# Performance work log

Hardware: AMD Instinct MI355X
Metric: run time of the kernel (lower is better)

## Reference

```python
import jax, jax.numpy as jnp
import numpy as np

N = 8192      # num_nodes (adj.shape[0])
CIN = 32
COUT = 32     # must equal CIN so wd = x @ wp @ x.T is (N, N)
CS = 4        # Chebyshev order, static operator
CD = 4        # Chebyshev order, dynamic operator


def setup_inputs() -> dict:
    key = jax.random.key(0)
    k1, k2, k3, k4, k5 = jax.random.split(key, 5)
    x = jax.random.normal(k1, (N, CIN), jnp.float32)
    # scale ws so its spectral radius is O(1); keeps the Chebyshev recurrence numerically tame
    ws = jax.random.normal(k2, (N, N), jnp.float32) * np.float32(1.0 / np.sqrt(N))
    # small scale on wp so wd = x wp x^T has O(1) entries
    wp = jax.random.normal(k3, (CIN, COUT), jnp.float32) * np.float32(1e-3)
    ts = jax.random.normal(k4, (CS, CIN, COUT), jnp.float32)
    td = jax.random.normal(k5, (CD, CIN, COUT), jnp.float32)
    return {"x": x, "ws": ws, "wp": wp, "ts": ts, "td": td}


def reference(x, ws, wp, ts, td):
    # Static operator: Chebyshev expansion T0 = I, T1 = ws, Tk = 2 ws T_{k-1} - T_{k-2}.
    # Run the recurrence on the propagated features y_k = T_k(ws) @ x  (N, cin)
    # instead of forming the (N, N) polynomial matrices -- same math, far less traffic.
    y0 = x                      # T0 @ x
    y1 = ws @ x                 # T1 @ x
    out = y0 @ ts[0]            # shared k=0 term (added into both branches, as in the source)
    out_s = out + y1 @ ts[1]
    for k in range(2, CS):
        y0, y1 = y1, 2.0 * (ws @ y1) - y0
        out_s = out_s + y1 @ ts[k]
    # Dynamic operator: data-dependent graph wd = x @ wp @ x.T  (N, N)
    wd = (x @ wp) @ x.T
    z0 = x
    z1 = wd @ x
    out_d = out + z1 @ td[1]
    for k in range(2, CD):
        z0, z1 = z1, 2.0 * (wd @ z1) - z0
        out_d = out_d + z1 @ td[k]
    # act_func is None in this configuration
    return out_s + out_d
```

## Files before the change

kernel.cpp:

```cpp
#include <hip/hip_runtime.h>
#include <hip/hip_bf16.h>


typedef __attribute__((ext_vector_type(8))) short short8;
typedef __attribute__((ext_vector_type(4))) float floatx4;

constexpr int NSPLIT = 8;

__device__ inline unsigned short f2bf(float f) {
    union { float f; unsigned u; } v; v.f = f;
    unsigned r = v.u + 0x7FFFu + ((v.u >> 16) & 1u);
    return (unsigned short)(r >> 16);
}

__device__ inline floatx4 ntload4(const float* p) {
    return __builtin_nontemporal_load((const floatx4*)p);
}

__global__ __launch_bounds__(256) void k_prep(const float* __restrict__ x,
                                              const float* __restrict__ wp,
                                              float* __restrict__ xp,
                                              float* __restrict__ Gpart,
                                              unsigned short* __restrict__ Vb) {
    __shared__ float sx[8192];
    __shared__ float swp[1024];
    __shared__ unsigned short st[32][264];
    const int t = threadIdx.x;
    const int n0 = blockIdx.x * 256;
    const floatx4* x4 = (const floatx4*)(x + (size_t)n0 * 32);
    floatx4* sx4 = (floatx4*)sx;
#pragma unroll
    for (int i = 0; i < 8; ++i) sx4[i * 256 + t] = x4[i * 256 + t];
    for (int i = t; i < 1024; i += 256) swp[i] = wp[i];
    __syncthreads();

    float row[32];
#pragma unroll
    for (int a = 0; a < 32; ++a) row[a] = sx[t * 32 + a];

    float* xpr = xp + (size_t)(n0 + t) * 32;
#pragma unroll
    for (int c = 0; c < 32; ++c) {
        float s = 0.f;
#pragma unroll
        for (int a = 0; a < 32; ++a) s += row[a] * swp[a * 32 + c];
        xpr[c] = s;
        st[c][t] = f2bf(row[c]);
    }

    const int a = t >> 3;
    const int b = 4 * (t & 7);
    float g0 = 0.f, g1 = 0.f, g2 = 0.f, g3 = 0.f;
    for (int i = 0; i < 256; ++i) {
        float va = sx[i * 32 + a];
        floatx4 vb = *(floatx4*)&sx[i * 32 + b];
        g0 += va * vb.x; g1 += va * vb.y; g2 += va * vb.z; g3 += va * vb.w;
    }
    floatx4 g = {g0, g1, g2, g3};
    *(floatx4*)&Gpart[(size_t)blockIdx.x * 1024 + (size_t)(a * 32 + b)] = g;

    __syncthreads();
    const int lane = t & 63, wv = t >> 6;
    const int l15 = lane & 15, l4 = lane >> 4;
    short8* Vb8 = (short8*)Vb;
#pragma unroll
    for (int q = 0; q < 4; ++q) {
        int idx = wv * 4 + q;
        int c8 = idx >> 1, h = idx & 1;
        short8 v = *(const short8*)&st[h * 16 + l15][c8 * 32 + l4 * 8];
        Vb8[((size_t)(n0 / 32 + c8) * 2 + h) * 64 + lane] = v;
    }
}

__global__ void k_coef(const float* __restrict__ Gpart, const float* __restrict__ wp,
                       const float* __restrict__ ts, const float* __restrict__ td,
                       float* __restrict__ Cx, float* __restrict__ Cxp) {
    __shared__ float G[1024], W[1024], H1[1024], H2[1024];
    __shared__ float swp[1024], td1[1024], td2[1024], td3[1024], ts0[1024];
    int t = threadIdx.x;
    int a = t >> 5, b = t & 31;
    float gs = 0.f;
    for (int p = 0; p < 32; ++p) gs += Gpart[p * 1024 + t];
    G[t] = gs; swp[t] = wp[t]; ts0[t] = ts[t];
    td1[t] = td[1024 + t]; td2[t] = td[2048 + t]; td3[t] = td[3072 + t];
    __syncthreads();
    float s = 0.f;
    for (int c = 0; c < 32; ++c) s += G[a * 32 + c] * swp[c * 32 + b];
    W[t] = s; __syncthreads();
    s = 0.f;
    for (int c = 0; c < 32; ++c) s += W[a * 32 + c] * G[c * 32 + b];
    H1[t] = s; __syncthreads();
    s = 0.f;
    for (int c = 0; c < 32; ++c) s += W[a * 32 + c] * H1[c * 32 + b];
    H2[t] = 2.f * s - G[t]; __syncthreads();
    s = 0.f;
    for (int c = 0; c < 32; ++c)
        s += G[a * 32 + c] * td1[c * 32 + b]
           + 2.f * H1[a * 32 + c] * td2[c * 32 + b]
           + (2.f * H2[a * 32 + c] - G[a * 32 + c]) * td3[c * 32 + b];
    Cxp[t] = s;
    Cx[t] = 2.f * ts0[t] - td2[t];
}

__global__ __launch_bounds__(256) void k_gemm1(const float* __restrict__ A,
                                               unsigned short* __restrict__ wsb,
                                               const unsigned short* __restrict__ Vb,
                                               float* __restrict__ Ypart) {
    __shared__ unsigned short sbuf[4][16 * 256];
    const int t = threadIdx.x;
    const int lane = t & 63;
    const int wv = t >> 6;
    const int l15 = lane & 15;
    const int l4 = lane >> 4;
    const int bx = blockIdx.x, by = blockIdx.y;
    const int k0 = by * 1024;
    const int kc0 = by * 32;
    const int rowbase = bx * 64 + wv * 16;

    unsigned short* wout =
        wsb + (((size_t)(bx * NSPLIT + by) * 8192) + (size_t)wv * 64 + lane) * 8;
    const short8* Vb8 = (const short8*)Vb;
    unsigned short* mybuf = sbuf[wv];
    const int wchunk = lane >> 1, whalf = lane & 1;

    floatx4 acc0 = {0.f, 0.f, 0.f, 0.f};
    floatx4 acc1 = {0.f, 0.f, 0.f, 0.f};

    for (int s = 0; s < 4; ++s) {
        const int ks = k0 + s * 256;
#pragma unroll
        for (int r = 0; r < 16; ++r) {
            floatx4 f = ntload4(A + (size_t)(rowbase + r) * 8192 + ks + lane * 4);
            ushort4 h;
            h.x = f2bf(f.x); h.y = f2bf(f.y); h.z = f2bf(f.z); h.w = f2bf(f.w);
            *(ushort4*)(mybuf + r * 256 + ((wchunk ^ r) * 8 + whalf * 4)) = h;
        }
#pragma unroll 4
        for (int kk = 0; kk < 8; ++kk) {
            short8 av = *(short8*)(mybuf + l15 * 256 + (((kk * 4 + l4) ^ l15) * 8));
            const int kc = kc0 + s * 8 + kk;
            short8 b0 = Vb8[((size_t)kc * 2 + 0) * 64 + lane];
            short8 b1 = Vb8[((size_t)kc * 2 + 1) * 64 + lane];
            *(short8*)(wout + (size_t)(s * 8 + kk) * 2048) = av;
            acc0 = __builtin_amdgcn_mfma_f32_16x16x32_bf16(av, b0, acc0, 0, 0, 0);
            acc1 = __builtin_amdgcn_mfma_f32_16x16x32_bf16(av, b1, acc1, 0, 0, 0);
        }
    }
    float* yp = Ypart + (size_t)by * 262144;
    const int row0 = bx * 64 + wv * 16 + l4 * 4;
#pragma unroll
    for (int r = 0; r < 4; ++r) {
        yp[(size_t)(row0 + r) * 32 + l15] = acc0[r];
        yp[(size_t)(row0 + r) * 32 + 16 + l15] = acc1[r];
    }
}

__global__ __launch_bounds__(256) void k_gemm2(const unsigned short* __restrict__ wsb,
                                               const unsigned short* __restrict__ Vb,
                                               float* __restrict__ Ypart) {
    const int t = threadIdx.x;
    const int lane = t & 63;
    const int wv = t >> 6;
    const int l15 = lane & 15;
    const int l4 = lane >> 4;
    const int bx = blockIdx.x, by = blockIdx.y;
    const int kc0 = by * 32;

    const short8* win = (const short8*)wsb
        + ((size_t)(bx * NSPLIT + by) * 8192) + (size_t)wv * 64 + lane;
    const short8* Vb8 = (const short8*)Vb;

    floatx4 acc0 = {0.f, 0.f, 0.f, 0.f};
    floatx4 acc1 = {0.f, 0.f, 0.f, 0.f};

#pragma unroll 8
    for (int c = 0; c < 32; ++c) {
        short8 av = win[(size_t)c * 256];
        short8 b0 = Vb8[((size_t)(kc0 + c) * 2 + 0) * 64 + lane];
        short8 b1 = Vb8[((size_t)(kc0 + c) * 2 + 1) * 64 + lane];
        acc0 = __builtin_amdgcn_mfma_f32_16x16x32_bf16(av, b0, acc0, 0, 0, 0);
        acc1 = __builtin_amdgcn_mfma_f32_16x16x32_bf16(av, b1, acc1, 0, 0, 0);
    }
    float* yp = Ypart + (size_t)by * 262144;
    const int row0 = bx * 64 + wv * 16 + l4 * 4;
#pragma unroll
    for (int r = 0; r < 4; ++r) {
        yp[(size_t)(row0 + r) * 32 + l15] = acc0[r];
        yp[(size_t)(row0 + r) * 32 + 16 + l15] = acc1[r];
    }
}

__global__ __launch_bounds__(256) void k_trans(const float* __restrict__ Ypart,
                                               const float* __restrict__ prev,
                                               float alpha, float beta,
                                               float* __restrict__ y,
                                               unsigned short* __restrict__ Vb) {
    __shared__ unsigned short st[32][264];
    const int t = threadIdx.x;
    const int n0 = blockIdx.x * 256;
    const size_t base4 = (size_t)n0 * 8;
    floatx4 r[8];
#pragma unroll
    for (int j = 0; j < 8; ++j) r[j] = {0.f, 0.f, 0.f, 0.f};
    for (int p = 0; p < NSPLIT; ++p) {
        const float* P = Ypart + (size_t)p * 262144;
#pragma unroll
        for (int j = 0; j < 8; ++j)
            r[j] += ntload4(P + (base4 + j * 256 + t) * 4);
    }
    const floatx4* prev4 = (const floatx4*)prev;
    floatx4* y4 = (floatx4*)y;
#pragma unroll
    for (int j = 0; j < 8; ++j) {
        floatx4 pv = prev4[base4 + j * 256 + t];
        floatx4 v;
        v.x = alpha * r[j].x + beta * pv.x;
        v.y = alpha * r[j].y + beta * pv.y;
        v.z = alpha * r[j].z + beta * pv.z;
        v.w = alpha * r[j].w + beta * pv.w;
        y4[base4 + j * 256 + t] = v;
        int q = j * 256 + t;
        int lr = q >> 3;
        int c4 = (q & 7) * 4;
        st[c4 + 0][lr] = f2bf(v.x);
        st[c4 + 1][lr] = f2bf(v.y);
        st[c4 + 2][lr] = f2bf(v.z);
        st[c4 + 3][lr] = f2bf(v.w);
    }
    __syncthreads();
    const int lane = t & 63, wv = t >> 6;
    const int l15 = lane & 15, l4 = lane >> 4;
    short8* Vb8 = (short8*)Vb;
#pragma unroll
    for (int q = 0; q < 4; ++q) {
        int idx = wv * 4 + q;
        int c8 = idx >> 1, h = idx & 1;
        short8 v = *(const short8*)&st[h * 16 + l15][c8 * 32 + l4 * 8];
        Vb8[((size_t)(n0 / 32 + c8) * 2 + h) * 64 + lane] = v;
    }
}

__global__ void k_final(const float* __restrict__ x, const float* __restrict__ xp,
                        const float* __restrict__ y1, const float* __restrict__ y2,
                        const float* __restrict__ y3, const float* __restrict__ Cx,
                        const float* __restrict__ Cxp, const float* __restrict__ ts,
                        float* __restrict__ out) {
    __shared__ float m0[1024], m1[1024], m2[1024], m3[1024], m4[1024];
    int t = threadIdx.x;
    for (int i = t; i < 1024; i += 256) {
        m0[i] = Cx[i]; m1[i] = Cxp[i];
        m2[i] = ts[1024 + i]; m3[i] = ts[2048 + i]; m4[i] = ts[3072 + i];
    }
    __syncthreads();
    int g = blockIdx.x * 256 + t;
    int n = g >> 5, c = g & 31;
    const float* xr  = x  + (size_t)n * 32;
    const float* xpr = xp + (size_t)n * 32;
    const float* y1r = y1 + (size_t)n * 32;
    const float* y2r = y2 + (size_t)n * 32;
    const float* y3r = y3 + (size_t)n * 32;
    float s = 0.f;
#pragma unroll
    for (int a = 0; a < 32; ++a) {
        s += xr[a]  * m0[a * 32 + c]
           + xpr[a] * m1[a * 32 + c]
           + y1r[a] * m2[a * 32 + c]
           + y2r[a] * m3[a * 32 + c]
           + y3r[a] * m4[a * 32 + c];
    }
    out[g] = s;
}

extern "C" void kernel_launch(void* const* d_in, const int* in_sizes, int n_in,
                              void* d_out, int out_size, void* d_ws, size_t ws_size,
                              hipStream_t stream) {
    const float* x  = (const float*)d_in[0];
    const float* ws = (const float*)d_in[1];
    const float* wp = (const float*)d_in[2];
    const float* ts = (const float*)d_in[3];
    const float* td = (const float*)d_in[4];
    float* out = (float*)d_out;

    char* w = (char*)d_ws;
    unsigned short* wsb = (unsigned short*)w;
    float* Ppart = (float*)(w + 134217728);
    float* xp  = Ppart + (size_t)NSPLIT * 262144;
    float* y1  = xp + 262144;
    float* y2  = y1 + 262144;
    float* y3  = y2 + 262144;
    unsigned short* Vb = (unsigned short*)(y3 + 262144);
    float* Gpart = (float*)(Vb + 262144);
    float* Cx  = Gpart + 32768;
    float* Cxp = Cx + 1024;

    dim3 gg(128, NSPLIT);
    k_prep<<<32, 256, 0, stream>>>(x, wp, xp, Gpart, Vb);
    k_coef<<<1, 1024, 0, stream>>>(Gpart, wp, ts, td, Cx, Cxp);
    k_gemm1<<<gg, 256, 0, stream>>>(ws, wsb, Vb, Ppart);
    k_trans<<<32, 256, 0, stream>>>(Ppart, x, 1.0f, 0.0f, y1, Vb);
    k_gemm2<<<gg, 256, 0, stream>>>(wsb, Vb, Ppart);
    k_trans<<<32, 256, 0, stream>>>(Ppart, x, 2.0f, -1.0f, y2, Vb);
    k_gemm2<<<gg, 256, 0, stream>>>(wsb, Vb, Ppart);
    k_trans<<<32, 256, 0, stream>>>(Ppart, y1, 2.0f, -1.0f, y3, Vb);

    k_final<<<1024, 256, 0, stream>>>(x, xp, y1, y2, y3, Cx, Cxp, ts, out);
}
```

Measured before the change: 481.6 us.

## Fuse pipeline into one cooperative persistent kernel holding ws tiles in registers

Replaces the nine-kernel sequence with a single cooperative kernel of 1024 blocks that converts its ws tile to bf16 once and keeps it in registers (32 short8 per lane) across all three propagation passes, separated by grid-wide syncs. This removes the 128 MB bf16 copy of ws written to and re-read from global memory, and removes the per-kernel launch gaps. It costs heavy register pressure at 4 blocks per CU, requires all 1024 blocks to be co-resident, and adds grid-sync latency. The old multi-kernel path is kept as a fallback if the cooperative launch fails.

```diff
diff --git a/kernel.cpp b/kernel.cpp
--- a/kernel.cpp
+++ b/kernel.cpp
@@ -1,6 +1,8 @@
 #include <hip/hip_runtime.h>
-#include <hip/hip_bf16.h>
-
+#include <hip/hip_cooperative_groups.h>
+
+
+namespace cg = cooperative_groups;
 
 typedef __attribute__((ext_vector_type(8))) short short8;
 typedef __attribute__((ext_vector_type(4))) float floatx4;
@@ -15,6 +17,235 @@
 
 __device__ inline floatx4 ntload4(const float* p) {
     return __builtin_nontemporal_load((const floatx4*)p);
+}
+
+struct __align__(16) SMem {
+    union {
+        unsigned short sbuf[4][16 * 256];
+        struct { float swp[1024]; unsigned short st[32][136]; } prep;
+        struct { float G[1024], W[1024], H1[1024], H2[1024]; } coef;
+        unsigned short st16[32][48];
+        float fin[5][1024];
+    };
+};
+
+__global__ __launch_bounds__(256, 4) void k_all(
+    const float* __restrict__ x, const float* __restrict__ ws,
+    const float* __restrict__ wp, const float* __restrict__ ts,
+    const float* __restrict__ td, float* __restrict__ out,
+    float* __restrict__ xp, float* __restrict__ y1,
+    float* __restrict__ y2, float* __restrict__ y3,
+    unsigned short* __restrict__ Vb0, unsigned short* __restrict__ Vb1,
+    unsigned short* __restrict__ Vb2, float* __restrict__ Yp,
+    float* __restrict__ Gpart, float* __restrict__ Cx, float* __restrict__ Cxp)
+{
+    cg::grid_group grid = cg::this_grid();
+    __shared__ SMem sm;
+    const int t = threadIdx.x;
+    const int lane = t & 63, wv = t >> 6, l15 = lane & 15, l4 = lane >> 4;
+    const int bid = blockIdx.x;
+    const int bx = bid >> 3, by = bid & 7;
+    const int k0 = by * 1024, kc0 = by * 32;
+    const int rowbase = bx * 64 + wv * 16;
+
+    if (bid < 64) {
+        const int n0 = bid * 128;
+        for (int i = t; i < 1024; i += 256) sm.prep.swp[i] = wp[i];
+        __syncthreads();
+        if (t < 128) {
+            const float* xr = x + (size_t)(n0 + t) * 32;
+            float row[32];
+#pragma unroll
+            for (int a = 0; a < 32; ++a) row[a] = xr[a];
+            float* xpr = xp + (size_t)(n0 + t) * 32;
+#pragma unroll
+            for (int c = 0; c < 32; ++c) {
+                float s = 0.f;
+#pragma unroll
+                for (int a = 0; a < 32; ++a) s += row[a] * sm.prep.swp[a * 32 + c];
+                xpr[c] = s;
+                sm.prep.st[c][t] = f2bf(row[c]);
+            }
+        }
+        {
+            const int a = t >> 3, b4 = 4 * (t & 7);
+            float g0 = 0.f, g1 = 0.f, g2 = 0.f, g3 = 0.f;
+            for (int i = 0; i < 128; ++i) {
+                float va = x[(size_t)(n0 + i) * 32 + a];
+                floatx4 vb = *(const floatx4*)&x[(size_t)(n0 + i) * 32 + b4];
+                g0 += va * vb.x; g1 += va * vb.y; g2 += va * vb.z; g3 += va * vb.w;
+            }
+            floatx4 g = {g0, g1, g2, g3};
+            *(floatx4*)&Gpart[(size_t)bid * 1024 + (size_t)(a * 32 + b4)] = g;
+        }
+        __syncthreads();
+        short8* Vb8 = (short8*)Vb0;
+#pragma unroll
+        for (int q = 0; q < 2; ++q) {
+            int idx = wv * 2 + q;
+            int c8 = idx >> 1, h = idx & 1;
+            short8 v = *(const short8*)&sm.prep.st[h * 16 + l15][c8 * 32 + l4 * 8];
+            Vb8[((size_t)(n0 / 32 + c8) * 2 + h) * 64 + lane] = v;
+        }
+        __syncthreads();
+    }
+
+    short8 wreg[32];
+    {
+        unsigned short* mybuf = sm.sbuf[wv];
+        const int wchunk = lane >> 1, whalf = lane & 1;
+#pragma unroll
+        for (int s = 0; s < 4; ++s) {
+            const int ks = k0 + s * 256;
+#pragma unroll
+            for (int r = 0; r < 16; ++r) {
+                floatx4 f = ntload4(ws + (size_t)(rowbase + r) * 8192 + ks + lane * 4);
+                ushort4 h;
+                h.x = f2bf(f.x); h.y = f2bf(f.y); h.z = f2bf(f.z); h.w = f2bf(f.w);
+                *(ushort4*)(mybuf + r * 256 + ((wchunk ^ r) * 8 + whalf * 4)) = h;
+            }
+#pragma unroll
+            for (int kk = 0; kk < 8; ++kk)
+                wreg[s * 8 + kk] = *(short8*)(mybuf + l15 * 256 + (((kk * 4 + l4) ^ l15) * 8));
+        }
+    }
+    grid.sync();
+
+#define DO_PASS(VBSRC, YDST)                                                          \
+    {                                                                                 \
+        const short8* Vb8_ = (const short8*)(VBSRC);                                  \
+        floatx4 acc0 = {0.f, 0.f, 0.f, 0.f};                                          \
+        floatx4 acc1 = {0.f, 0.f, 0.f, 0.f};                                          \
+        _Pragma("unroll")                                                             \
+        for (int c = 0; c < 32; ++c) {                                                \
+            short8 b0 = Vb8_[((size_t)(kc0 + c) * 2 + 0) * 64 + lane];                \
+            short8 b1 = Vb8_[((size_t)(kc0 + c) * 2 + 1) * 64 + lane];                \
+            acc0 = __builtin_amdgcn_mfma_f32_16x16x32_bf16(wreg[c], b0, acc0, 0, 0, 0); \
+            acc1 = __builtin_amdgcn_mfma_f32_16x16x32_bf16(wreg[c], b1, acc1, 0, 0, 0); \
+        }                                                                             \
+        float* yp_ = (YDST) + (size_t)by * 262144;                                    \
+        const int row0_ = bx * 64 + wv * 16 + l4 * 4;                                 \
+        _Pragma("unroll")                                                             \
+        for (int r = 0; r < 4; ++r) {                                                 \
+            yp_[(size_t)(row0_ + r) * 32 + l15] = acc0[r];                            \
+            yp_[(size_t)(row0_ + r) * 32 + 16 + l15] = acc1[r];                       \
+        }                                                                             \
+    }
+
+#define DO_TRANS(YSRC, PREV, ALPHA, BETA, YOUT, VBE, EMIT)                            \
+    if (bid >= 1 && bid <= 256) {                                                     \
+        const int kc_ = bid - 1;                                                      \
+        const int row_ = t >> 3, c4_ = (t & 7) * 4;                                   \
+        const size_t base_ = ((size_t)kc_ * 32 + row_) * 32 + c4_;                    \
+        floatx4 racc = {0.f, 0.f, 0.f, 0.f};                                          \
+        _Pragma("unroll")                                                             \
+        for (int p = 0; p < NSPLIT; ++p) {                                            \
+            floatx4 v_ = ntload4((YSRC) + (size_t)p * 262144 + base_);                \
+            racc.x += v_.x; racc.y += v_.y; racc.z += v_.z; racc.w += v_.w;           \
+        }                                                                             \
+        floatx4 pv = *(const floatx4*)((PREV) + base_);                               \
+        floatx4 v;                                                                    \
+        v.x = (ALPHA) * racc.x + (BETA) * pv.x;                                       \
+        v.y = (ALPHA) * racc.y + (BETA) * pv.y;                                       \
+        v.z = (ALPHA) * racc.z + (BETA) * pv.z;                                       \
+        v.w = (ALPHA) * racc.w + (BETA) * pv.w;                                       \
+        *(floatx4*)((YOUT) + base_) = v;                                              \
+        if (EMIT) {                                                                   \
+            sm.st16[c4_ + 0][row_] = f2bf(v.x);                                       \
+            sm.st16[c4_ + 1][row_] = f2bf(v.y);                                       \
+            sm.st16[c4_ + 2][row_] = f2bf(v.z);                                       \
+            sm.st16[c4_ + 3][row_] = f2bf(v.w);                                       \
+            __syncthreads();                                                          \
+            if (wv < 2) {                                                             \
+                short8 vv = *(const short8*)&sm.st16[wv * 16 + l15][l4 * 8];          \
+                ((short8*)(VBE))[((size_t)kc_ * 2 + wv) * 64 + lane] = vv;            \
+            }                                                                         \
+        }                                                                             \
+    }
+
+    DO_PASS(Vb0, Yp)
+    grid.sync();
+    DO_TRANS(Yp, x, 1.f, 0.f, y1, Vb1, 1)
+    if (bid == 0) {
+#pragma unroll
+        for (int j = 0; j < 4; ++j) {
+            int e = t + j * 256;
+            float g = 0.f;
+            for (int p = 0; p < 64; ++p) g += Gpart[p * 1024 + e];
+            sm.coef.G[e] = g;
+        }
+        __syncthreads();
+#pragma unroll
+        for (int j = 0; j < 4; ++j) {
+            int e = t + j * 256, a = e >> 5, b = e & 31;
+            float s = 0.f;
+            for (int c = 0; c < 32; ++c) s += sm.coef.G[a * 32 + c] * wp[c * 32 + b];
+            sm.coef.W[e] = s;
+        }
+        __syncthreads();
+#pragma unroll
+        for (int j = 0; j < 4; ++j) {
+            int e = t + j * 256, a = e >> 5, b = e & 31;
+            float s = 0.f;
+            for (int c = 0; c < 32; ++c) s += sm.coef.W[a * 32 + c] * sm.coef.G[c * 32 + b];
+            sm.coef.H1[e] = s;
+        }
+        __syncthreads();
+#pragma unroll
+        for (int j = 0; j < 4; ++j) {
+            int e = t + j * 256, a = e >> 5, b = e & 31;
+            float s = 0.f;
+            for (int c = 0; c < 32; ++c) s += sm.coef.W[a * 32 + c] * sm.coef.H1[c * 32 + b];
+            sm.coef.H2[e] = 2.f * s - sm.coef.G[e];
+        }
+        __syncthreads();
+#pragma unroll
+        for (int j = 0; j < 4; ++j) {
+            int e = t + j * 256, a = e >> 5, b = e & 31;
+            float s = 0.f;
+            for (int c = 0; c < 32; ++c)
+                s += sm.coef.G[a * 32 + c] * td[1024 + c * 32 + b]
+                   + 2.f * sm.coef.H1[a * 32 + c] * td[2048 + c * 32 + b]
+                   + (2.f * sm.coef.H2[a * 32 + c] - sm.coef.G[a * 32 + c]) * td[3072 + c * 32 + b];
+            Cxp[e] = s;
+            Cx[e] = 2.f * ts[e] - td[2048 + e];
+        }
+    }
+    grid.sync();
+    DO_PASS(Vb1, Yp + 2097152)
+    grid.sync();
+    DO_TRANS(Yp + 2097152, x, 2.f, -1.f, y2, Vb2, 1)
+    grid.sync();
+    DO_PASS(Vb2, Yp + 4194304)
+    grid.sync();
+    DO_TRANS(Yp + 4194304, y1, 2.f, -1.f, y3, Vb2, 0)
+    grid.sync();
+
+    for (int i = t; i < 1024; i += 256) {
+        sm.fin[0][i] = Cx[i]; sm.fin[1][i] = Cxp[i];
+        sm.fin[2][i] = ts[1024 + i]; sm.fin[3][i] = ts[2048 + i]; sm.fin[4][i] = ts[3072 + i];
+    }
+    __syncthreads();
+    {
+        const int n = bid * 8 + (t >> 5), c = t & 31;
+        const float* xr  = x  + (size_t)n * 32;
+        const float* xpr = xp + (size_t)n * 32;
+        const float* y1r = y1 + (size_t)n * 32;
+        const float* y2r = y2 + (size_t)n * 32;
+        const float* y3r = y3 + (size_t)n * 32;
+        float s = 0.f;
+#pragma unroll
+        for (int a = 0; a < 32; ++a) {
+            s += xr[a]  * sm.fin[0][a * 32 + c]
+               + xpr[a] * sm.fin[1][a * 32 + c]
+               + y1r[a] * sm.fin[2][a * 32 + c]
+               + y2r[a] * sm.fin[3][a * 32 + c]
+               + y3r[a] * sm.fin[4][a * 32 + c];
+        }
+        out[(size_t)n * 32 + c] = s;
+    }
+#undef DO_PASS
+#undef DO_TRANS
 }
 
 __global__ __launch_bounds__(256) void k_prep(const float* __restrict__ x,
@@ -33,11 +264,9 @@
     for (int i = 0; i < 8; ++i) sx4[i * 256 + t] = x4[i * 256 + t];
     for (int i = t; i < 1024; i += 256) swp[i] = wp[i];
     __syncthreads();
-
     float row[32];
 #pragma unroll
     for (int a = 0; a < 32; ++a) row[a] = sx[t * 32 + a];
-
     float* xpr = xp + (size_t)(n0 + t) * 32;
 #pragma unroll
     for (int c = 0; c < 32; ++c) {
@@ -47,7 +276,6 @@
         xpr[c] = s;
         st[c][t] = f2bf(row[c]);
     }
-
     const int a = t >> 3;
     const int b = 4 * (t & 7);
     float g0 = 0.f, g1 = 0.f, g2 = 0.f, g3 = 0.f;
@@ -58,7 +286,6 @@
     }
     floatx4 g = {g0, g1, g2, g3};
     *(floatx4*)&Gpart[(size_t)blockIdx.x * 1024 + (size_t)(a * 32 + b)] = g;
-
     __syncthreads();
     const int lane = t & 63, wv = t >> 6;
     const int l15 = lane & 15, l4 = lane >> 4;
@@ -116,16 +343,13 @@
     const int k0 = by * 1024;
     const int kc0 = by * 32;
     const int rowbase = bx * 64 + wv * 16;
-
     unsigned short* wout =
         wsb + (((size_t)(bx * NSPLIT + by) * 8192) + (size_t)wv * 64 + lane) * 8;
     const short8* Vb8 = (const short8*)Vb;
     unsigned short* mybuf = sbuf[wv];
     const int wchunk = lane >> 1, whalf = lane & 1;
-
     floatx4 acc0 = {0.f, 0.f, 0.f, 0.f};
     floatx4 acc1 = {0.f, 0.f, 0.f, 0.f};
-
     for (int s = 0; s < 4; ++s) {
         const int ks = k0 + s * 256;
 #pragma unroll
@@ -165,14 +389,11 @@
     const int l4 = lane >> 4;
     const int bx = blockIdx.x, by = blockIdx.y;
     const int kc0 = by * 32;
-
     const short8* win = (const short8*)wsb
         + ((size_t)(bx * NSPLIT + by) * 8192) + (size_t)wv * 64 + lane;
     const short8* Vb8 = (const short8*)Vb;
-
     floatx4 acc0 = {0.f, 0.f, 0.f, 0.f};
     floatx4 acc1 = {0.f, 0.f, 0.f, 0.f};
-
 #pragma unroll 8
     for (int c = 0; c < 32; ++c) {
         short8 av = win[(size_t)c * 256];
@@ -282,26 +503,46 @@
     float* out = (float*)d_out;
 
     char* w = (char*)d_ws;
+
+    float* Yp = (float*)w;
+    float* xp = Yp + 3 * 2097152;
+    float* y1 = xp + 262144;
+    float* y2 = y1 + 262144;
+    float* y3 = y2 + 262144;
+    unsigned short* Vb0 = (unsigned short*)(y3 + 262144);
+    unsigned short* Vb1 = Vb0 + 262144;
+    unsigned short* Vb2 = Vb1 + 262144;
+    float* Gpart = (float*)(Vb2 + 262144);
+    float* Cx  = Gpart + 65536;
+    float* Cxp = Cx + 1024;
+
+    void* args[] = {(void*)&x, (void*)&ws, (void*)&wp, (void*)&ts, (void*)&td,
+                    (void*)&out, (void*)&xp, (void*)&y1, (void*)&y2, (void*)&y3,
+                    (void*)&Vb0, (void*)&Vb1, (void*)&Vb2, (void*)&Yp,
+                    (void*)&Gpart, (void*)&Cx, (void*)&Cxp};
+    hipError_t err = hipLaunchCooperativeKernel((void*)k_all, dim3(1024), dim3(256),
+                                                args, 0, stream);
+    if (err == hipSuccess) return;
+
     unsigned short* wsb = (unsigned short*)w;
     float* Ppart = (float*)(w + 134217728);
-    float* xp  = Ppart + (size_t)NSPLIT * 262144;
-    float* y1  = xp + 262144;
-    float* y2  = y1 + 262144;
-    float* y3  = y2 + 262144;
-    unsigned short* Vb = (unsigned short*)(y3 + 262144);
-    float* Gpart = (float*)(Vb + 262144);
-    float* Cx  = Gpart + 32768;
-    float* Cxp = Cx + 1024;
+    float* fxp = Ppart + (size_t)NSPLIT * 262144;
+    float* fy1 = fxp + 262144;
+    float* fy2 = fy1 + 262144;
+    float* fy3 = fy2 + 262144;
+    unsigned short* fVb = (unsigned short*)(fy3 + 262144);
+    float* fGpart = (float*)(fVb + 262144);
+    float* fCx  = fGpart + 32768;
+    float* fCxp = fCx + 1024;
 
     dim3 gg(128, NSPLIT);
-    k_prep<<<32, 256, 0, stream>>>(x, wp, xp, Gpart, Vb);
-    k_coef<<<1, 1024, 0, stream>>>(Gpart, wp, ts, td, Cx, Cxp);
-    k_gemm1<<<gg, 256, 0, stream>>>(ws, wsb, Vb, Ppart);
-    k_trans<<<32, 256, 0, stream>>>(Ppart, x, 1.0f, 0.0f, y1, Vb);
-    k_gemm2<<<gg, 256, 0, stream>>>(wsb, Vb, Ppart);
-    k_trans<<<32, 256, 0, stream>>>(Ppart, x, 2.0f, -1.0f, y2, Vb);
-    k_gemm2<<<gg, 256, 0, stream>>>(wsb, Vb, Ppart);
-    k_trans<<<32, 256, 0, stream>>>(Ppart, y1, 2.0f, -1.0f, y3, Vb);
-
-    k_final<<<1024, 256, 0, stream>>>(x, xp, y1, y2, y3, Cx, Cxp, ts, out);
-}
+    k_prep<<<32, 256, 0, stream>>>(x, wp, fxp, fGpart, fVb);
+    k_coef<<<1, 1024, 0, stream>>>(fGpart, wp, ts, td, fCx, fCxp);
+    k_gemm1<<<gg, 256, 0, stream>>>(ws, wsb, fVb, Ppart);
+    k_trans<<<32, 256, 0, stream>>>(Ppart, x, 1.0f, 0.0f, fy1, fVb);
+    k_gemm2<<<gg, 256, 0, stream>>>(wsb, fVb, Ppart);
+    k_trans<<<32, 256, 0, stream>>>(Ppart, x, 2.0f, -1.0f, fy2, fVb);
+    k_gemm2<<<gg, 256, 0, stream>>>(wsb, fVb, Ppart);
+    k_trans<<<32, 256, 0, stream>>>(Ppart, fy1, 2.0f, -1.0f, fy3, fVb);
+    k_final<<<1024, 256, 0, stream>>>(x, fxp, fy1, fy2, fy3, fCx, fCxp, ts, out);
+}
```

Result: slower. 1.356 ms (+181.5%).

## Fuse split-K GEMMs with in-block reduction, recurrence update and final projection

Applied to the files above, without the earlier changes.

Replaces the separate GEMM, partial-sum transpose, coefficient and final kernels with one templated kernel per Chebyshev step. Each 1024-thread block owns 32 rows and does the full K split across its 16 waves, reducing partial sums in shared memory instead of writing 8 partial buffers to global memory and re-reading them. The coefficient computation runs in an extra block of the first launch, and the output projection is fused into the last step. This cuts kernel launches and global partial-sum traffic. In exchange, the grid is smaller (256 large blocks) and the shared-memory footprint per block is heavier.

```diff
diff --git a/kernel.cpp b/kernel.cpp
--- a/kernel.cpp
+++ b/kernel.cpp
@@ -1,11 +1,8 @@
 #include <hip/hip_runtime.h>
-#include <hip/hip_bf16.h>
 
 
 typedef __attribute__((ext_vector_type(8))) short short8;
 typedef __attribute__((ext_vector_type(4))) float floatx4;
-
-constexpr int NSPLIT = 8;
 
 __device__ inline unsigned short f2bf(float f) {
     union { float f; unsigned u; } v; v.f = f;
@@ -33,11 +30,9 @@
     for (int i = 0; i < 8; ++i) sx4[i * 256 + t] = x4[i * 256 + t];
     for (int i = t; i < 1024; i += 256) swp[i] = wp[i];
     __syncthreads();
-
     float row[32];
 #pragma unroll
     for (int a = 0; a < 32; ++a) row[a] = sx[t * 32 + a];
-
     float* xpr = xp + (size_t)(n0 + t) * 32;
 #pragma unroll
     for (int c = 0; c < 32; ++c) {
@@ -47,7 +42,6 @@
         xpr[c] = s;
         st[c][t] = f2bf(row[c]);
     }
-
     const int a = t >> 3;
     const int b = 4 * (t & 7);
     float g0 = 0.f, g1 = 0.f, g2 = 0.f, g3 = 0.f;
@@ -58,7 +52,6 @@
     }
     floatx4 g = {g0, g1, g2, g3};
     *(floatx4*)&Gpart[(size_t)blockIdx.x * 1024 + (size_t)(a * 32 + b)] = g;
-
     __syncthreads();
     const int lane = t & 63, wv = t >> 6;
     const int l15 = lane & 15, l4 = lane >> 4;
@@ -72,203 +65,158 @@
     }
 }
 
-__global__ void k_coef(const float* __restrict__ Gpart, const float* __restrict__ wp,
-                       const float* __restrict__ ts, const float* __restrict__ td,
-                       float* __restrict__ Cx, float* __restrict__ Cxp) {
-    __shared__ float G[1024], W[1024], H1[1024], H2[1024];
-    __shared__ float swp[1024], td1[1024], td2[1024], td3[1024], ts0[1024];
-    int t = threadIdx.x;
-    int a = t >> 5, b = t & 31;
-    float gs = 0.f;
-    for (int p = 0; p < 32; ++p) gs += Gpart[p * 1024 + t];
-    G[t] = gs; swp[t] = wp[t]; ts0[t] = ts[t];
-    td1[t] = td[1024 + t]; td2[t] = td[2048 + t]; td3[t] = td[3072 + t];
-    __syncthreads();
-    float s = 0.f;
-    for (int c = 0; c < 32; ++c) s += G[a * 32 + c] * swp[c * 32 + b];
-    W[t] = s; __syncthreads();
-    s = 0.f;
-    for (int c = 0; c < 32; ++c) s += W[a * 32 + c] * G[c * 32 + b];
-    H1[t] = s; __syncthreads();
-    s = 0.f;
-    for (int c = 0; c < 32; ++c) s += W[a * 32 + c] * H1[c * 32 + b];
-    H2[t] = 2.f * s - G[t]; __syncthreads();
-    s = 0.f;
-    for (int c = 0; c < 32; ++c)
-        s += G[a * 32 + c] * td1[c * 32 + b]
-           + 2.f * H1[a * 32 + c] * td2[c * 32 + b]
-           + (2.f * H2[a * 32 + c] - G[a * 32 + c]) * td3[c * 32 + b];
-    Cxp[t] = s;
-    Cx[t] = 2.f * ts0[t] - td2[t];
-}
-
-__global__ __launch_bounds__(256) void k_gemm1(const float* __restrict__ A,
-                                               unsigned short* __restrict__ wsb,
-                                               const unsigned short* __restrict__ Vb,
-                                               float* __restrict__ Ypart) {
-    __shared__ unsigned short sbuf[4][16 * 256];
+struct __align__(16) ChebSM {
+    union {
+        float red[16 * 512];
+        struct { float G[1024], W[1024], H1[1024], H2[1024]; } coef;
+        float fin[5 * 1024];
+    };
+    union {
+        unsigned short st16[32][48];
+        struct { float y3s[32][33], xs[32][33], xps[32][33],
+                       y1s[32][33], y2s[32][33]; } f;
+    };
+};
+
+template <int MODE>
+__global__ __launch_bounds__(1024, 4) void k_cheb(
+    const float* __restrict__ wsf, unsigned short* __restrict__ wsb,
+    const unsigned short* __restrict__ VbIn,
+    const float* __restrict__ prev, float alpha, float beta,
+    float* __restrict__ yout, unsigned short* __restrict__ VbOut,
+    const float* __restrict__ Gpart, const float* __restrict__ wp,
+    const float* __restrict__ ts, const float* __restrict__ td,
+    float* __restrict__ Cx, float* __restrict__ Cxp,
+    const float* __restrict__ x, const float* __restrict__ xp,
+    const float* __restrict__ y1, const float* __restrict__ y2,
+    float* __restrict__ out)
+{
+    __shared__ ChebSM sm;
     const int t = threadIdx.x;
-    const int lane = t & 63;
-    const int wv = t >> 6;
-    const int l15 = lane & 15;
-    const int l4 = lane >> 4;
-    const int bx = blockIdx.x, by = blockIdx.y;
-    const int k0 = by * 1024;
-    const int kc0 = by * 32;
-    const int rowbase = bx * 64 + wv * 16;
-
-    unsigned short* wout =
-        wsb + (((size_t)(bx * NSPLIT + by) * 8192) + (size_t)wv * 64 + lane) * 8;
-    const short8* Vb8 = (const short8*)Vb;
-    unsigned short* mybuf = sbuf[wv];
-    const int wchunk = lane >> 1, whalf = lane & 1;
+    const int bid = blockIdx.x;
+
+    if (MODE == 1 && bid == 256) {
+        const int a = t >> 5, b = t & 31;
+        float g = 0.f;
+        for (int p = 0; p < 32; ++p) g += Gpart[p * 1024 + t];
+        sm.coef.G[t] = g;
+        __syncthreads();
+        float s = 0.f;
+        for (int c = 0; c < 32; ++c) s += sm.coef.G[a * 32 + c] * wp[c * 32 + b];
+        sm.coef.W[t] = s;
+        __syncthreads();
+        s = 0.f;
+        for (int c = 0; c < 32; ++c) s += sm.coef.W[a * 32 + c] * sm.coef.G[c * 32 + b];
+        sm.coef.H1[t] = s;
+        __syncthreads();
+        s = 0.f;
+        for (int c = 0; c < 32; ++c) s += sm.coef.W[a * 32 + c] * sm.coef.H1[c * 32 + b];
+        sm.coef.H2[t] = 2.f * s - sm.coef.G[t];
+        __syncthreads();
+        s = 0.f;
+        for (int c = 0; c < 32; ++c)
+            s += sm.coef.G[a * 32 + c] * td[1024 + c * 32 + b]
+               + 2.f * sm.coef.H1[a * 32 + c] * td[2048 + c * 32 + b]
+               + (2.f * sm.coef.H2[a * 32 + c] - sm.coef.G[a * 32 + c]) * td[3072 + c * 32 + b];
+        Cxp[t] = s;
+        Cx[t] = 2.f * ts[t] - td[2048 + t];
+        return;
+    }
+
+    const int lane = t & 63, wv = t >> 6;
+    const int l15 = lane & 15, l4 = lane >> 4;
+    const int rg = wv >> 3, ks = wv & 7;
+    const int n0 = bid * 32;
 
     floatx4 acc0 = {0.f, 0.f, 0.f, 0.f};
     floatx4 acc1 = {0.f, 0.f, 0.f, 0.f};
-
-    for (int s = 0; s < 4; ++s) {
-        const int ks = k0 + s * 256;
-#pragma unroll
-        for (int r = 0; r < 16; ++r) {
-            floatx4 f = ntload4(A + (size_t)(rowbase + r) * 8192 + ks + lane * 4);
-            ushort4 h;
-            h.x = f2bf(f.x); h.y = f2bf(f.y); h.z = f2bf(f.z); h.w = f2bf(f.w);
-            *(ushort4*)(mybuf + r * 256 + ((wchunk ^ r) * 8 + whalf * 4)) = h;
-        }
+    const short8* Vb8 = (const short8*)VbIn;
+
+    if (MODE == 1) {
+        const float* arow = wsf + (size_t)(n0 + rg * 16 + l15) * 8192 + ks * 1024 + l4 * 8;
+        short8* wout = (short8*)wsb + (((size_t)(bid * 2 + rg) * 8 + ks) * 32) * 64 + lane;
 #pragma unroll 4
-        for (int kk = 0; kk < 8; ++kk) {
-            short8 av = *(short8*)(mybuf + l15 * 256 + (((kk * 4 + l4) ^ l15) * 8));
-            const int kc = kc0 + s * 8 + kk;
-            short8 b0 = Vb8[((size_t)kc * 2 + 0) * 64 + lane];
-            short8 b1 = Vb8[((size_t)kc * 2 + 1) * 64 + lane];
-            *(short8*)(wout + (size_t)(s * 8 + kk) * 2048) = av;
+        for (int c = 0; c < 32; ++c) {
+            floatx4 f0 = ntload4(arow + c * 32);
+            floatx4 f1 = ntload4(arow + c * 32 + 4);
+            short8 av;
+            av[0] = (short)f2bf(f0.x); av[1] = (short)f2bf(f0.y);
+            av[2] = (short)f2bf(f0.z); av[3] = (short)f2bf(f0.w);
+            av[4] = (short)f2bf(f1.x); av[5] = (short)f2bf(f1.y);
+            av[6] = (short)f2bf(f1.z); av[7] = (short)f2bf(f1.w);
+            const int gkc = ks * 32 + c;
+            short8 b0 = Vb8[((size_t)gkc * 2 + 0) * 64 + lane];
+            short8 b1 = Vb8[((size_t)gkc * 2 + 1) * 64 + lane];
+            wout[(size_t)c * 64] = av;
             acc0 = __builtin_amdgcn_mfma_f32_16x16x32_bf16(av, b0, acc0, 0, 0, 0);
             acc1 = __builtin_amdgcn_mfma_f32_16x16x32_bf16(av, b1, acc1, 0, 0, 0);
         }
-    }
-    float* yp = Ypart + (size_t)by * 262144;
-    const int row0 = bx * 64 + wv * 16 + l4 * 4;
-#pragma unroll
-    for (int r = 0; r < 4; ++r) {
-        yp[(size_t)(row0 + r) * 32 + l15] = acc0[r];
-        yp[(size_t)(row0 + r) * 32 + 16 + l15] = acc1[r];
-    }
-}
-
-__global__ __launch_bounds__(256) void k_gemm2(const unsigned short* __restrict__ wsb,
-                                               const unsigned short* __restrict__ Vb,
-                                               float* __restrict__ Ypart) {
-    const int t = threadIdx.x;
-    const int lane = t & 63;
-    const int wv = t >> 6;
-    const int l15 = lane & 15;
-    const int l4 = lane >> 4;
-    const int bx = blockIdx.x, by = blockIdx.y;
-    const int kc0 = by * 32;
-
-    const short8* win = (const short8*)wsb
-        + ((size_t)(bx * NSPLIT + by) * 8192) + (size_t)wv * 64 + lane;
-    const short8* Vb8 = (const short8*)Vb;
-
-    floatx4 acc0 = {0.f, 0.f, 0.f, 0.f};
-    floatx4 acc1 = {0.f, 0.f, 0.f, 0.f};
-
+    } else {
+        const short8* win = (const short8*)wsb + (((size_t)(bid * 2 + rg) * 8 + ks) * 32) * 64 + lane;
 #pragma unroll 8
-    for (int c = 0; c < 32; ++c) {
-        short8 av = win[(size_t)c * 256];
-        short8 b0 = Vb8[((size_t)(kc0 + c) * 2 + 0) * 64 + lane];
-        short8 b1 = Vb8[((size_t)(kc0 + c) * 2 + 1) * 64 + lane];
-        acc0 = __builtin_amdgcn_mfma_f32_16x16x32_bf16(av, b0, acc0, 0, 0, 0);
-        acc1 = __builtin_amdgcn_mfma_f32_16x16x32_bf16(av, b1, acc1, 0, 0, 0);
-    }
-    float* yp = Ypart + (size_t)by * 262144;
-    const int row0 = bx * 64 + wv * 16 + l4 * 4;
-#pragma unroll
-    for (int r = 0; r < 4; ++r) {
-        yp[(size_t)(row0 + r) * 32 + l15] = acc0[r];
-        yp[(size_t)(row0 + r) * 32 + 16 + l15] = acc1[r];
-    }
-}
-
-__global__ __launch_bounds__(256) void k_trans(const float* __restrict__ Ypart,
-                                               const float* __restrict__ prev,
-                                               float alpha, float beta,
-                                               float* __restrict__ y,
-                                               unsigned short* __restrict__ Vb) {
-    __shared__ unsigned short st[32][264];
-    const int t = threadIdx.x;
-    const int n0 = blockIdx.x * 256;
-    const size_t base4 = (size_t)n0 * 8;
-    floatx4 r[8];
-#pragma unroll
-    for (int j = 0; j < 8; ++j) r[j] = {0.f, 0.f, 0.f, 0.f};
-    for (int p = 0; p < NSPLIT; ++p) {
-        const float* P = Ypart + (size_t)p * 262144;
-#pragma unroll
-        for (int j = 0; j < 8; ++j)
-            r[j] += ntload4(P + (base4 + j * 256 + t) * 4);
-    }
-    const floatx4* prev4 = (const floatx4*)prev;
-    floatx4* y4 = (floatx4*)y;
-#pragma unroll
-    for (int j = 0; j < 8; ++j) {
-        floatx4 pv = prev4[base4 + j * 256 + t];
-        floatx4 v;
-        v.x = alpha * r[j].x + beta * pv.x;
-        v.y = alpha * r[j].y + beta * pv.y;
-        v.z = alpha * r[j].z + beta * pv.z;
-        v.w = alpha * r[j].w + beta * pv.w;
-        y4[base4 + j * 256 + t] = v;
-        int q = j * 256 + t;
-        int lr = q >> 3;
-        int c4 = (q & 7) * 4;
-        st[c4 + 0][lr] = f2bf(v.x);
-        st[c4 + 1][lr] = f2bf(v.y);
-        st[c4 + 2][lr] = f2bf(v.z);
-        st[c4 + 3][lr] = f2bf(v.w);
+        for (int c = 0; c < 32; ++c) {
+            short8 av = win[(size_t)c * 64];
+            const int gkc = ks * 32 + c;
+            short8 b0 = Vb8[((size_t)gkc * 2 + 0) * 64 + lane];
+            short8 b1 = Vb8[((size_t)gkc * 2 + 1) * 64 + lane];
+            acc0 = __builtin_amdgcn_mfma_f32_16x16x32_bf16(av, b0, acc0, 0, 0, 0);
+            acc1 = __builtin_amdgcn_mfma_f32_16x16x32_bf16(av, b1, acc1, 0, 0, 0);
+        }
+    }
+
+    {
+        const int base = (rg * 8 + ks) * 512;
+#pragma unroll
+        for (int r = 0; r < 4; ++r) {
+            sm.red[base + (l4 * 4 + r) * 32 + l15]      = acc0[r];
+            sm.red[base + (l4 * 4 + r) * 32 + 16 + l15] = acc1[r];
+        }
     }
     __syncthreads();
-    const int lane = t & 63, wv = t >> 6;
-    const int l15 = lane & 15, l4 = lane >> 4;
-    short8* Vb8 = (short8*)Vb;
-#pragma unroll
-    for (int q = 0; q < 4; ++q) {
-        int idx = wv * 4 + q;
-        int c8 = idx >> 1, h = idx & 1;
-        short8 v = *(const short8*)&st[h * 16 + l15][c8 * 32 + l4 * 8];
-        Vb8[((size_t)(n0 / 32 + c8) * 2 + h) * 64 + lane] = v;
-    }
-}
-
-__global__ void k_final(const float* __restrict__ x, const float* __restrict__ xp,
-                        const float* __restrict__ y1, const float* __restrict__ y2,
-                        const float* __restrict__ y3, const float* __restrict__ Cx,
-                        const float* __restrict__ Cxp, const float* __restrict__ ts,
-                        float* __restrict__ out) {
-    __shared__ float m0[1024], m1[1024], m2[1024], m3[1024], m4[1024];
-    int t = threadIdx.x;
-    for (int i = t; i < 1024; i += 256) {
-        m0[i] = Cx[i]; m1[i] = Cxp[i];
-        m2[i] = ts[1024 + i]; m3[i] = ts[2048 + i]; m4[i] = ts[3072 + i];
-    }
-    __syncthreads();
-    int g = blockIdx.x * 256 + t;
-    int n = g >> 5, c = g & 31;
-    const float* xr  = x  + (size_t)n * 32;
-    const float* xpr = xp + (size_t)n * 32;
-    const float* y1r = y1 + (size_t)n * 32;
-    const float* y2r = y2 + (size_t)n * 32;
-    const float* y3r = y3 + (size_t)n * 32;
+
+    const int rr = t >> 5, cc = t & 31;
+    const int rrg = rr >> 4, rrl = rr & 15;
     float s = 0.f;
 #pragma unroll
-    for (int a = 0; a < 32; ++a) {
-        s += xr[a]  * m0[a * 32 + c]
-           + xpr[a] * m1[a * 32 + c]
-           + y1r[a] * m2[a * 32 + c]
-           + y2r[a] * m3[a * 32 + c]
-           + y3r[a] * m4[a * 32 + c];
-    }
-    out[g] = s;
+    for (int k = 0; k < 8; ++k) s += sm.red[(rrg * 8 + k) * 512 + rrl * 32 + cc];
+    const float pv = prev[(size_t)(n0 + rr) * 32 + cc];
+    const float v = alpha * s + beta * pv;
+
+    if (MODE != 3) {
+        yout[(size_t)(n0 + rr) * 32 + cc] = v;
+        sm.st16[cc][rr] = f2bf(v);
+        __syncthreads();
+        if (t < 128) {
+            const int h = t >> 6, ln = t & 63;
+            const int hl15 = ln & 15, hl4 = ln >> 4;
+            short8 v8 = *(const short8*)&sm.st16[h * 16 + hl15][hl4 * 8];
+            ((short8*)VbOut)[((size_t)bid * 2 + h) * 64 + ln] = v8;
+        }
+    } else {
+        sm.f.y3s[rr][cc] = v;
+        __syncthreads();
+        sm.fin[t]        = Cx[t];
+        sm.fin[1024 + t] = Cxp[t];
+        sm.fin[2048 + t] = ts[1024 + t];
+        sm.fin[3072 + t] = ts[2048 + t];
+        sm.fin[4096 + t] = ts[3072 + t];
+        const size_t gidx = (size_t)(n0 + rr) * 32 + cc;
+        sm.f.xs[rr][cc]  = x[gidx];
+        sm.f.xps[rr][cc] = xp[gidx];
+        sm.f.y1s[rr][cc] = y1[gidx];
+        sm.f.y2s[rr][cc] = y2[gidx];
+        __syncthreads();
+        float o = 0.f;
+#pragma unroll
+        for (int a = 0; a < 32; ++a) {
+            o += sm.f.xs[rr][a]  * sm.fin[a * 32 + cc]
+               + sm.f.xps[rr][a] * sm.fin[1024 + a * 32 + cc]
+               + sm.f.y1s[rr][a] * sm.fin[2048 + a * 32 + cc]
+               + sm.f.y2s[rr][a] * sm.fin[3072 + a * 32 + cc]
+               + sm.f.y3s[rr][a] * sm.fin[4096 + a * 32 + cc];
+        }
+        out[gidx] = o;
+    }
 }
 
 extern "C" void kernel_launch(void* const* d_in, const int* in_sizes, int n_in,
@@ -283,25 +231,25 @@
 
     char* w = (char*)d_ws;
     unsigned short* wsb = (unsigned short*)w;
-    float* Ppart = (float*)(w + 134217728);
-    float* xp  = Ppart + (size_t)NSPLIT * 262144;
+    float* xp  = (float*)(w + 134217728);
     float* y1  = xp + 262144;
     float* y2  = y1 + 262144;
-    float* y3  = y2 + 262144;
-    unsigned short* Vb = (unsigned short*)(y3 + 262144);
-    float* Gpart = (float*)(Vb + 262144);
+    unsigned short* Vb0 = (unsigned short*)(y2 + 262144);
+    unsigned short* Vb1 = Vb0 + 262144;
+    unsigned short* Vb2 = Vb1 + 262144;
+    float* Gpart = (float*)(Vb2 + 262144);
     float* Cx  = Gpart + 32768;
     float* Cxp = Cx + 1024;
 
-    dim3 gg(128, NSPLIT);
-    k_prep<<<32, 256, 0, stream>>>(x, wp, xp, Gpart, Vb);
-    k_coef<<<1, 1024, 0, stream>>>(Gpart, wp, ts, td, Cx, Cxp);
-    k_gemm1<<<gg, 256, 0, stream>>>(ws, wsb, Vb, Ppart);
-    k_trans<<<32, 256, 0, stream>>>(Ppart, x, 1.0f, 0.0f, y1, Vb);
-    k_gemm2<<<gg, 256, 0, stream>>>(wsb, Vb, Ppart);
-    k_trans<<<32, 256, 0, stream>>>(Ppart, x, 2.0f, -1.0f, y2, Vb);
-    k_gemm2<<<gg, 256, 0, stream>>>(wsb, Vb, Ppart);
-    k_trans<<<32, 256, 0, stream>>>(Ppart, y1, 2.0f, -1.0f, y3, Vb);
-
-    k_final<<<1024, 256, 0, stream>>>(x, xp, y1, y2, y3, Cx, Cxp, ts, out);
-}
+    k_prep<<<32, 256, 0, stream>>>(x, wp, xp, Gpart, Vb0);
+
+    k_cheb<1><<<257, 1024, 0, stream>>>(ws, wsb, Vb0, x, 1.0f, 0.0f, y1, Vb1,
+                                        Gpart, wp, ts, td, Cx, Cxp,
+                                        x, xp, y1, y2, out);
+    k_cheb<2><<<256, 1024, 0, stream>>>(nullptr, wsb, Vb1, x, 2.0f, -1.0f, y2, Vb2,
+                                        nullptr, nullptr, nullptr, nullptr, nullptr, nullptr,
+                                        nullptr, nullptr, nullptr, nullptr, nullptr);
+    k_cheb<3><<<256, 1024, 0, stream>>>(nullptr, wsb, Vb2, y1, 2.0f, -1.0f, nullptr, nullptr,
+                                        nullptr, nullptr, ts, nullptr, Cx, Cxp,
+                                        x, xp, y1, y2, out);
+}
```

Result: faster. 456.2 us (-5.3%).
